# Kernel tuning notes

Measured on AMD Instinct MI355X. Metric: run time of the kernel, lower is better.

## Reference

```python
import jax, jax.numpy as jnp
import numpy as np

N_NODES = 100000
N_EDGES = 3200000
N_GRAPHS = 128
IN_DIM = 4
HID = 64
BN_EPS = 1e-5


def setup_inputs() -> dict:
    key = jax.random.key(0)
    ks = jax.random.split(key, 24)
    x = jax.random.normal(ks[0], (N_NODES, IN_DIM), dtype=jnp.float32)
    edge_index = jax.random.randint(ks[1], (2, N_EDGES), 0, N_NODES, dtype=jnp.int32)
    batch_ids = jnp.sort(jax.random.randint(ks[2], (N_NODES,), 0, N_GRAPHS, dtype=jnp.int32))

    def lin(k, out_d, in_d):
        s = 1.0 / np.sqrt(in_d)
        return jax.random.uniform(k, (out_d, in_d), jnp.float32, -s, s)

    inp = {
        'x': x, 'edge_index': edge_index, 'batch_ids': batch_ids,
        # SAGEConv i: out = lin_l(mean_neighbors) + lin_r(x_self); bias lives in lin_l
        'w1l': lin(ks[3], HID, IN_DIM), 'b1': jnp.zeros((HID,), jnp.float32), 'w1r': lin(ks[4], HID, IN_DIM),
        'bn1_g': jnp.ones((HID,), jnp.float32), 'bn1_b': jnp.zeros((HID,), jnp.float32),
        'w2l': lin(ks[5], HID, HID), 'b2': jnp.zeros((HID,), jnp.float32), 'w2r': lin(ks[6], HID, HID),
        'bn2_g': jnp.ones((HID,), jnp.float32), 'bn2_b': jnp.zeros((HID,), jnp.float32),
        'w3l': lin(ks[7], HID, HID), 'b3': jnp.zeros((HID,), jnp.float32), 'w3r': lin(ks[8], HID, HID),
        'bn3_g': jnp.ones((HID,), jnp.float32), 'bn3_b': jnp.zeros((HID,), jnp.float32),
        'fc1_w': lin(ks[9], 64, HID), 'fc1_b': jnp.zeros((64,), jnp.float32),
        'fc2_w': lin(ks[10], 2, 64), 'fc2_b': jnp.zeros((2,), jnp.float32),
    }
    return inp


def _sage(x, src, dst, deg_inv, wl, bl, wr):
    # mean-aggregate neighbor messages (source -> target), then two small GEMMs
    msum = jax.ops.segment_sum(x[src], dst, num_segments=N_NODES)  # [N, d]
    agg = msum * deg_inv[:, None]
    return agg @ wl.T + bl + x @ wr.T


def _bn(x, g, b):
    # BatchNorm1d in training mode: batch stats over node dim, biased variance
    m = jnp.mean(x, axis=0)
    v = jnp.mean((x - m) ** 2, axis=0)
    return (x - m) * jax.lax.rsqrt(v + BN_EPS) * g + b


def reference(x, edge_index, batch_ids,
              w1l, b1, w1r, bn1_g, bn1_b,
              w2l, b2, w2r, bn2_g, bn2_b,
              w3l, b3, w3r, bn3_g, bn3_b,
              fc1_w, fc1_b, fc2_w, fc2_b):
    src, dst = edge_index[0], edge_index[1]
    deg = jax.ops.segment_sum(jnp.ones((src.shape[0],), x.dtype), dst, num_segments=N_NODES)
    deg_inv = 1.0 / jnp.maximum(deg, 1.0)

    h = jax.nn.relu(_bn(_sage(x, src, dst, deg_inv, w1l, b1, w1r), bn1_g, bn1_b))
    h = jax.nn.relu(_bn(_sage(h, src, dst, deg_inv, w2l, b2, w2r), bn2_g, bn2_b))
    h = jax.nn.relu(_bn(_sage(h, src, dst, deg_inv, w3l, b3, w3r), bn3_g, bn3_b))

    # global_mean_pool over graphs
    gsum = jax.ops.segment_sum(h, batch_ids, num_segments=N_GRAPHS)
    gcnt = jax.ops.segment_sum(jnp.ones((h.shape[0],), h.dtype), batch_ids, num_segments=N_GRAPHS)
    pooled = gsum / jnp.maximum(gcnt, 1.0)[:, None]

    # MLP head (dropout = identity at inference)
    hid = jax.nn.relu(pooled @ fc1_w.T + fc1_b)
    return hid @ fc2_w.T + fc2_b
```

## Files before the change

kernel.cpp:

```cpp
#include <hip/hip_runtime.h>
#include <hip/hip_fp16.h>

#define NN 100000
#define NE 3200000
#define NG 128
#define BN_EPS 1e-5f

#define NBUK 782
#define BSHIFT 7
#define BCAP 6144

#define GRID_SG 1024
#define PBMAX 2048
#define PSLICE 8

typedef _Float16 h2v __attribute__((ext_vector_type(2)));
typedef unsigned int u32x2 __attribute__((ext_vector_type(2)));
typedef unsigned int u32x4 __attribute__((ext_vector_type(4)));


__global__ void __launch_bounds__(512) k_scatter(
    const int* __restrict__ src, const int* __restrict__ dst,
    int* __restrict__ slab_cursor, unsigned int* __restrict__ slab, int E) {
    __shared__ int hist[NBUK + 2];
    __shared__ int cbase[NBUK + 2];
    int tid = threadIdx.x;
    int eBeg = blockIdx.x * 12500;
    int eEnd = min(eBeg + 12500, E);

    for (int t = tid; t < NBUK; t += 512) hist[t] = 0;
    __syncthreads();
    for (int e = eBeg + tid; e < eEnd; e += 512) {
        int b = dst[e] >> BSHIFT;
        atomicAdd(&hist[b], 1);
    }
    __syncthreads();
    for (int t = tid; t < NBUK; t += 512) {
        int c = hist[t];
        cbase[t] = (c > 0) ? atomicAdd(&slab_cursor[t], c) : 0;
    }
    __syncthreads();
    for (int t = tid; t < NBUK; t += 512) hist[t] = 0;
    __syncthreads();
    for (int e = eBeg + tid; e < eEnd; e += 512) {
        int d = dst[e];
        int b = d >> BSHIFT;
        int r = atomicAdd(&hist[b], 1);
        int pos = cbase[b] + r;
        if (pos < BCAP) slab[(size_t)b * BCAP + pos] = ((unsigned)src[e] << BSHIFT) | (unsigned)(d & 127);
    }
}

__global__ void __launch_bounds__(512) k_bucket_csr(
    const unsigned int* __restrict__ slab, const int* __restrict__ slab_cursor,
    int* __restrict__ row_ptr,
    float* __restrict__ deg_inv, int* __restrict__ csr_src,
    const float* __restrict__ x, const float* __restrict__ w1l,
    const float* __restrict__ b1, const float* __restrict__ w1r,
    __half* __restrict__ hp16, float* __restrict__ part) {
    __shared__ int lds_csr[BCAP];
    __shared__ int red[512];
    __shared__ int sdeg[128];
    __shared__ int sscan[128];
    __shared__ int slcur[128];
    __shared__ float swl[256], swr[256], sb1[64];
    __shared__ float ssum[64], ssq[64];
    int tid = threadIdx.x;
    int b = blockIdx.x;
    int lo = b << BSHIFT;
    int cnt = min(slab_cursor[b], BCAP);
    const unsigned int* sl = slab + (size_t)b * BCAP;

    int partial = 0;
    for (int j = tid; j < b; j += 512) partial += min(slab_cursor[j], BCAP);
    red[tid] = partial;
    __syncthreads();
    for (int off = 256; off > 0; off >>= 1) {
        if (tid < off) red[tid] += red[tid + off];
        __syncthreads();
    }
    int base = red[0];
    if (b == NBUK - 1 && tid == 0) row_ptr[NN] = base + cnt;

    if (tid < 256) { swl[tid] = w1l[tid]; swr[tid] = w1r[tid]; }
    if (tid < 64)  { sb1[tid] = b1[tid]; ssum[tid] = 0.f; ssq[tid] = 0.f; }
    if (tid < 128) sdeg[tid] = 0;
    __syncthreads();

    unsigned int myv[12];
    int mycount = 0;
    for (int k = tid; k < cnt; k += 512) myv[mycount++] = sl[k];
#pragma unroll
    for (int j = 0; j < 12; j++)
        if (j < mycount) atomicAdd(&sdeg[myv[j] & 127], 1);
    __syncthreads();
    int v = (tid < 128) ? sdeg[tid] : 0;
    if (tid < 128) sscan[tid] = v;
    __syncthreads();
    for (int off = 1; off < 128; off <<= 1) {
        int add = 0;
        if (tid < 128 && tid >= off) add = sscan[tid - off];
        __syncthreads();
        if (tid < 128) sscan[tid] += add;
        __syncthreads();
    }
    if (tid < 128) {
        int excl = sscan[tid] - v;
        int n = lo + tid;
        if (n < NN) {
            row_ptr[n] = base + excl;
            deg_inv[n] = 1.0f / fmaxf((float)v, 1.0f);
        }
        slcur[tid] = excl;
    }
    __syncthreads();
#pragma unroll
    for (int j = 0; j < 12; j++)
        if (j < mycount) {
            unsigned int p = myv[j];
            int pos = atomicAdd(&slcur[p & 127], 1);
            lds_csr[pos] = (int)(p >> BSHIFT);
        }
    __syncthreads();
    for (int k = tid; k < cnt; k += 512) csr_src[base + k] = lds_csr[k];

    int i = tid >> 2, c = tid & 3;
    int n = lo + i;
    bool valid = (n < NN);
    int dhi = sscan[i];
    int dlo = dhi - sdeg[i];
    const float4* x4 = (const float4*)x;
    float4 acc = make_float4(0.f, 0.f, 0.f, 0.f);
    int k = dlo + c;
    for (; k + 12 < dhi; k += 16) {
        int s0 = lds_csr[k], s1 = lds_csr[k + 4], s2 = lds_csr[k + 8], s3 = lds_csr[k + 12];
        float4 v0 = x4[s0];
        float4 v1 = x4[s1];
        float4 v2 = x4[s2];
        float4 v3 = x4[s3];
        acc.x += v0.x + v1.x + v2.x + v3.x;
        acc.y += v0.y + v1.y + v2.y + v3.y;
        acc.z += v0.z + v1.z + v2.z + v3.z;
        acc.w += v0.w + v1.w + v2.w + v3.w;
    }
    for (; k < dhi; k += 4) {
        int s = lds_csr[k];
        float4 xv = x4[s];
        acc.x += xv.x; acc.y += xv.y; acc.z += xv.z; acc.w += xv.w;
    }
#pragma unroll
    for (int m = 1; m <= 2; m <<= 1) {
        acc.x += __shfl_xor(acc.x, m);
        acc.y += __shfl_xor(acc.y, m);
        acc.z += __shfl_xor(acc.z, m);
        acc.w += __shfl_xor(acc.w, m);
    }
    float dv = 1.0f / fmaxf((float)sdeg[i], 1.0f);
    float ax = acc.x * dv, ay = acc.y * dv, az = acc.z * dv, aw = acc.w * dv;
    float4 xs = valid ? x4[n] : make_float4(0.f, 0.f, 0.f, 0.f);

#pragma unroll
    for (int m4 = 0; m4 < 4; m4++) {
        float4 o = make_float4(0.f, 0.f, 0.f, 0.f);
        float* op = &o.x;
        if (valid) {
#pragma unroll
            for (int t = 0; t < 4; t++) {
                int j = c * 16 + m4 * 4 + t;
                float s = sb1[j];
                s += ax * swl[j * 4 + 0] + ay * swl[j * 4 + 1] + az * swl[j * 4 + 2] + aw * swl[j * 4 + 3];
                s += xs.x * swr[j * 4 + 0] + xs.y * swr[j * 4 + 1] + xs.z * swr[j * 4 + 2] + xs.w * swr[j * 4 + 3];
                op[t] = s;
            }
            h2v p0 = h2v{(_Float16)o.x, (_Float16)o.y};
            h2v p1 = h2v{(_Float16)o.z, (_Float16)o.w};
            u32x2 w;
            w.x = *(unsigned int*)&p0;
            w.y = *(unsigned int*)&p1;
            __builtin_nontemporal_store(w, (u32x2*)hp16 + (size_t)n * 16 + c * 4 + m4);
        }
        float4 q = make_float4(o.x * o.x, o.y * o.y, o.z * o.z, o.w * o.w);
#pragma unroll
        for (int m = 4; m <= 32; m <<= 1) {
            o.x += __shfl_xor(o.x, m); o.y += __shfl_xor(o.y, m);
            o.z += __shfl_xor(o.z, m); o.w += __shfl_xor(o.w, m);
            q.x += __shfl_xor(q.x, m); q.y += __shfl_xor(q.y, m);
            q.z += __shfl_xor(q.z, m); q.w += __shfl_xor(q.w, m);
        }
        if ((tid & 63) < 4) {
            int jb = c * 16 + m4 * 4;
            atomicAdd(&ssum[jb + 0], o.x); atomicAdd(&ssum[jb + 1], o.y);
            atomicAdd(&ssum[jb + 2], o.z); atomicAdd(&ssum[jb + 3], o.w);
            atomicAdd(&ssq[jb + 0], q.x);  atomicAdd(&ssq[jb + 1], q.y);
            atomicAdd(&ssq[jb + 2], q.z);  atomicAdd(&ssq[jb + 3], q.w);
        }
    }
    __syncthreads();
    if (tid < 64) {
        part[(2 * tid) * PBMAX + blockIdx.x]     = ssum[tid];
        part[(2 * tid + 1) * PBMAX + blockIdx.x] = ssq[tid];
    }
}

__global__ void __launch_bounds__(512, 8) k_sage(
    const __half* __restrict__ h_in, const float* __restrict__ sbv_in,
    const int* __restrict__ row_ptr,
    const int* __restrict__ csr_src, const float* __restrict__ deg_inv,
    const float* __restrict__ wl, const float* __restrict__ bl,
    const float* __restrict__ wr, __half* __restrict__ hp16,
    float* __restrict__ part) {
    __shared__ h2v wl2s[32][68];
    __shared__ h2v wr2s[32][68];
    __shared__ h2v tAh[32][36];
    __shared__ h2v tXh[32][36];
    __shared__ float ssum[64], ssq[64];
    int tid = threadIdx.x;
    for (int idx = tid; idx < 2048; idx += 512) {
        int j = idx & 63, kk = idx >> 6;
        float2 l = ((const float2*)wl)[j * 32 + kk];
        float2 r = ((const float2*)wr)[j * 32 + kk];
        wl2s[kk][j] = h2v{(_Float16)l.x, (_Float16)l.y};
        wr2s[kk][j] = h2v{(_Float16)r.x, (_Float16)r.y};
    }
    if (tid < 64) { ssum[tid] = 0.f; ssq[tid] = 0.f; }
    __syncthreads();

    int g = tid & 15, ni = tid >> 4;
    h2v sch0 = h2v{(_Float16)sbv_in[4 * g + 0], (_Float16)sbv_in[4 * g + 1]};
    h2v sch1 = h2v{(_Float16)sbv_in[4 * g + 2], (_Float16)sbv_in[4 * g + 3]};
    h2v bih0 = h2v{(_Float16)sbv_in[64 + 4 * g + 0], (_Float16)sbv_in[64 + 4 * g + 1]};
    h2v bih1 = h2v{(_Float16)sbv_in[64 + 4 * g + 2], (_Float16)sbv_in[64 + 4 * g + 3]};
    h2v hz = h2v{(_Float16)0.f, (_Float16)0.f};

    const uint2* tbl = (const uint2*)h_in;
    const int ntiles = NN / 32;

#define BN_ACC_H(vv) { \
        h2v a0 = *(h2v*)&vv.x, a1 = *(h2v*)&vv.y; \
        hacc0 += __builtin_elementwise_max(a0 * sch0 + bih0, hz); \
        hacc1 += __builtin_elementwise_max(a1 * sch1 + bih1, hz); }

    for (int tile = blockIdx.x; tile < ntiles; tile += GRID_SG) {
        int n = tile * 32 + ni;
        float ax = 0.f, ay = 0.f, az = 0.f, aw = 0.f;
        int r0 = row_ptr[n], r1 = row_ptr[n + 1];
        int e = r0;
        for (; e + 8 <= r1; e += 8) {
            int s0 = csr_src[e],     s1 = csr_src[e + 1], s2 = csr_src[e + 2], s3 = csr_src[e + 3];
            int s4 = csr_src[e + 4], s5 = csr_src[e + 5], s6 = csr_src[e + 6], s7 = csr_src[e + 7];
            uint2 v0 = tbl[(size_t)s0 * 16 + g];
            uint2 v1 = tbl[(size_t)s1 * 16 + g];
            uint2 v2 = tbl[(size_t)s2 * 16 + g];
            uint2 v3 = tbl[(size_t)s3 * 16 + g];
            uint2 v4 = tbl[(size_t)s4 * 16 + g];
            uint2 v5 = tbl[(size_t)s5 * 16 + g];
            uint2 v6 = tbl[(size_t)s6 * 16 + g];
            uint2 v7 = tbl[(size_t)s7 * 16 + g];
            h2v hacc0 = hz, hacc1 = hz;
            BN_ACC_H(v0) BN_ACC_H(v1) BN_ACC_H(v2) BN_ACC_H(v3)
            BN_ACC_H(v4) BN_ACC_H(v5) BN_ACC_H(v6) BN_ACC_H(v7)
            ax += (float)hacc0.x; ay += (float)hacc0.y;
            az += (float)hacc1.x; aw += (float)hacc1.y;
        }
        for (; e < r1; ++e) {
            int s = csr_src[e];
            uint2 vv = tbl[(size_t)s * 16 + g];
            h2v a0 = *(h2v*)&vv.x, a1 = *(h2v*)&vv.y;
            a0 = __builtin_elementwise_max(a0 * sch0 + bih0, hz);
            a1 = __builtin_elementwise_max(a1 * sch1 + bih1, hz);
            ax += (float)a0.x; ay += (float)a0.y; az += (float)a1.x; aw += (float)a1.y;
        }
        float di = deg_inv[n];
        uint2 rsv = tbl[(size_t)n * 16 + g];
        h2v xs0h = __builtin_elementwise_max(*(h2v*)&rsv.x * sch0 + bih0, hz);
        h2v xs1h = __builtin_elementwise_max(*(h2v*)&rsv.y * sch1 + bih1, hz);
        ax *= di; ay *= di; az *= di; aw *= di;
        tAh[ni][2 * g]     = h2v{(_Float16)ax, (_Float16)ay};
        tAh[ni][2 * g + 1] = h2v{(_Float16)az, (_Float16)aw};
        tXh[ni][2 * g]     = xs0h;
        tXh[ni][2 * g + 1] = xs1h;
        __syncthreads();

        float4 o = ((const float4*)bl)[g];
#pragma unroll 4
        for (int kk = 0; kk < 32; kk++) {
            h2v a2 = tAh[ni][kk];
            h2v x2 = tXh[ni][kk];
            h2v l0 = wl2s[kk][4 * g + 0], l1 = wl2s[kk][4 * g + 1];
            h2v l2 = wl2s[kk][4 * g + 2], l3 = wl2s[kk][4 * g + 3];
            h2v r0v = wr2s[kk][4 * g + 0], r1v = wr2s[kk][4 * g + 1];
            h2v r2v = wr2s[kk][4 * g + 2], r3v = wr2s[kk][4 * g + 3];
#if __has_builtin(__builtin_amdgcn_fdot2)
            o.x = __builtin_amdgcn_fdot2(a2, l0, o.x, false);
            o.y = __builtin_amdgcn_fdot2(a2, l1, o.y, false);
            o.z = __builtin_amdgcn_fdot2(a2, l2, o.z, false);
            o.w = __builtin_amdgcn_fdot2(a2, l3, o.w, false);
            o.x = __builtin_amdgcn_fdot2(x2, r0v, o.x, false);
            o.y = __builtin_amdgcn_fdot2(x2, r1v, o.y, false);
            o.z = __builtin_amdgcn_fdot2(x2, r2v, o.z, false);
            o.w = __builtin_amdgcn_fdot2(x2, r3v, o.w, false);
#else
            float b0 = (float)a2.x, b1 = (float)a2.y, x0 = (float)x2.x, x1 = (float)x2.y;
            o.x += b0 * (float)l0.x + b1 * (float)l0.y + x0 * (float)r0v.x + x1 * (float)r0v.y;
            o.y += b0 * (float)l1.x + b1 * (float)l1.y + x0 * (float)r1v.x + x1 * (float)r1v.y;
            o.z += b0 * (float)l2.x + b1 * (float)l2.y + x0 * (float)r2v.x + x1 * (float)r2v.y;
            o.w += b0 * (float)l3.x + b1 * (float)l3.y + x0 * (float)r3v.x + x1 * (float)r3v.y;
#endif
        }
        {
            h2v p0 = h2v{(_Float16)o.x, (_Float16)o.y};
            h2v p1 = h2v{(_Float16)o.z, (_Float16)o.w};
            u32x2 w;
            w.x = *(unsigned int*)&p0;
            w.y = *(unsigned int*)&p1;
            __builtin_nontemporal_store(w, (u32x2*)hp16 + (size_t)n * 16 + g);
        }

        float4 qv = make_float4(o.x * o.x, o.y * o.y, o.z * o.z, o.w * o.w);
#pragma unroll
        for (int m = 16; m <= 32; m <<= 1) {
            o.x += __shfl_xor(o.x, m); o.y += __shfl_xor(o.y, m);
            o.z += __shfl_xor(o.z, m); o.w += __shfl_xor(o.w, m);
            qv.x += __shfl_xor(qv.x, m); qv.y += __shfl_xor(qv.y, m);
            qv.z += __shfl_xor(qv.z, m); qv.w += __shfl_xor(qv.w, m);
        }
        if ((tid & 48) == 0) {
            atomicAdd(&ssum[4 * g + 0], o.x); atomicAdd(&ssum[4 * g + 1], o.y);
            atomicAdd(&ssum[4 * g + 2], o.z); atomicAdd(&ssum[4 * g + 3], o.w);
            atomicAdd(&ssq[4 * g + 0], qv.x);  atomicAdd(&ssq[4 * g + 1], qv.y);
            atomicAdd(&ssq[4 * g + 2], qv.z);  atomicAdd(&ssq[4 * g + 3], qv.w);
        }
        __syncthreads();
    }
#undef BN_ACC_H
    if (tid < 64) {
        part[(2 * tid) * PBMAX + blockIdx.x]     = ssum[tid];
        part[(2 * tid + 1) * PBMAX + blockIdx.x] = ssq[tid];
    }
}

__global__ void k_reduce_sb(const float* __restrict__ part, int PB,
                            const float* __restrict__ gamma, const float* __restrict__ beta,
                            float* __restrict__ sbv, int N) {
    int c = blockIdx.x;
    float s = 0.f, q = 0.f;
    for (int b = threadIdx.x; b < PB; b += 256) {
        s += part[(2 * c) * PBMAX + b];
        q += part[(2 * c + 1) * PBMAX + b];
    }
    __shared__ float rs[256], rq[256];
    rs[threadIdx.x] = s;
    rq[threadIdx.x] = q;
    __syncthreads();
    for (int off = 128; off > 0; off >>= 1) {
        if (threadIdx.x < off) {
            rs[threadIdx.x] += rs[threadIdx.x + off];
            rq[threadIdx.x] += rq[threadIdx.x + off];
        }
        __syncthreads();
    }
    if (threadIdx.x == 0) {
        float m = rs[0] / (float)N;
        float var = rq[0] / (float)N - m * m;
        float sc = gamma[c] * rsqrtf(var + BN_EPS);
        sbv[c]      = sc;
        sbv[64 + c] = beta[c] - m * sc;
    }
}

__global__ void __launch_bounds__(256) k_pool_partial(
    const __half* __restrict__ hp16, const float* __restrict__ sbv,
    const int* __restrict__ batch, float* __restrict__ pooled_part, int N) {
    __shared__ float ssc[64], sbi[64];
    __shared__ float sm[256];
    if (threadIdx.x < 64) {
        ssc[threadIdx.x] = sbv[threadIdx.x];
        sbi[threadIdx.x] = sbv[64 + threadIdx.x];
    }
    __syncthreads();
    int gph = blockIdx.x >> 3;
    int slice = blockIdx.x & 7;
    int lo = 0, hi = N;
    while (lo < hi) { int mid = (lo + hi) >> 1; if (batch[mid] < gph) lo = mid + 1; else hi = mid; }
    int start = lo;
    hi = N;
    while (lo < hi) { int mid = (lo + hi) >> 1; if (batch[mid] < gph + 1) lo = mid + 1; else hi = mid; }
    int end = lo;

    int c = threadIdx.x & 63, w = threadIdx.x >> 6;
    float s = 0.f;
    for (int r = start + slice * 4 + w; r < end; r += 32)
        s += fmaxf(__half2float(hp16[(size_t)r * 64 + c]) * ssc[c] + sbi[c], 0.f);
    sm[threadIdx.x] = s;
    __syncthreads();
    if (threadIdx.x < 64) {
        float t = sm[c] + sm[64 + c] + sm[128 + c] + sm[192 + c];
        pooled_part[(size_t)(gph * PSLICE + slice) * 64 + c] = t;
    }
}

__global__ void __launch_bounds__(64) k_head(
    const float* __restrict__ pooled_part, const int* __restrict__ batch,
    const float* __restrict__ fc1w, const float* __restrict__ fc1b,
    const float* __restrict__ fc2w, const float* __restrict__ fc2b,
    float* __restrict__ out, int N) {
    __shared__ float pl[64], hid[64];
    int gph = blockIdx.x;
    int j = threadIdx.x;
    int lo = 0, hi = N;
    while (lo < hi) { int mid = (lo + hi) >> 1; if (batch[mid] < gph) lo = mid + 1; else hi = mid; }
    int start = lo;
    hi = N;
    while (lo < hi) { int mid = (lo + hi) >> 1; if (batch[mid] < gph + 1) lo = mid + 1; else hi = mid; }
    int cnt = lo - start;

    float t = 0.f;
#pragma unroll
    for (int s = 0; s < PSLICE; s++) t += pooled_part[(size_t)(gph * PSLICE + s) * 64 + j];
    pl[j] = t / fmaxf((float)cnt, 1.0f);
    __syncthreads();
    float v = fc1b[j];
    for (int k = 0; k < 64; k++) v += pl[k] * fc1w[j * 64 + k];
    hid[j] = fmaxf(v, 0.f);
    __syncthreads();
    if (j < 2) {
        float o = fc2b[j];
        for (int k = 0; k < 64; k++) o += hid[k] * fc2w[j * 64 + k];
        out[gph * 2 + j] = o;
    }
}

extern "C" void kernel_launch(void* const* d_in, const int* in_sizes, int n_in,
                              void* d_out, int out_size, void* d_ws, size_t ws_size,
                              hipStream_t stream) {
    const float* x    = (const float*)d_in[0];
    const int* ei     = (const int*)d_in[1];
    const int* batch  = (const int*)d_in[2];
    const float* w1l  = (const float*)d_in[3];
    const float* b1   = (const float*)d_in[4];
    const float* w1r  = (const float*)d_in[5];
    const float* bn1g = (const float*)d_in[6];
    const float* bn1b = (const float*)d_in[7];
    const float* w2l  = (const float*)d_in[8];
    const float* b2   = (const float*)d_in[9];
    const float* w2r  = (const float*)d_in[10];
    const float* bn2g = (const float*)d_in[11];
    const float* bn2b = (const float*)d_in[12];
    const float* w3l  = (const float*)d_in[13];
    const float* b3   = (const float*)d_in[14];
    const float* w3r  = (const float*)d_in[15];
    const float* bn3g = (const float*)d_in[16];
    const float* bn3b = (const float*)d_in[17];
    const float* fc1w = (const float*)d_in[18];
    const float* fc1b = (const float*)d_in[19];
    const float* fc2w = (const float*)d_in[20];
    const float* fc2b = (const float*)d_in[21];
    float* out = (float*)d_out;

    const int N = NN, E = NE;
    const int* srcp = ei;
    const int* dstp = ei + E;

    char* ws = (char*)d_ws;
    size_t off = 0;
    auto alloc = [&](size_t bytes) -> char* {
        char* p = ws + off;
        off += (bytes + 255) & ~(size_t)255;
        return p;
    };
    int* csr_src       = (int*)alloc(sizeof(int) * E);
    __half* hpA        = (__half*)alloc(sizeof(__half) * N * 64);
    __half* hpB        = (__half*)alloc(sizeof(__half) * N * 64);
    unsigned int* slab = (unsigned int*)alloc(sizeof(unsigned int) * (size_t)NBUK * BCAP);
    int* slab_cursor   = (int*)alloc(sizeof(int) * NBUK);
    int* row_ptr       = (int*)alloc(sizeof(int) * (N + 1));
    float* deg_inv     = (float*)alloc(sizeof(float) * N);
    float* part        = (float*)alloc(sizeof(float) * 128 * PBMAX);
    float* sbv         = (float*)alloc(sizeof(float) * 128);
    float* pooled_part = (float*)alloc(sizeof(float) * NG * PSLICE * 64);

    hipMemsetAsync(slab_cursor, 0, sizeof(int) * NBUK, stream);

    k_scatter<<<256, 512, 0, stream>>>(srcp, dstp, slab_cursor, slab, E);
    k_bucket_csr<<<NBUK, 512, 0, stream>>>(slab, slab_cursor, row_ptr, deg_inv,
                                           csr_src, x, w1l, b1, w1r, hpA, part);
    k_reduce_sb<<<64, 256, 0, stream>>>(part, NBUK, bn1g, bn1b, sbv, N);

    k_sage<<<GRID_SG, 512, 0, stream>>>(hpA, sbv, row_ptr, csr_src, deg_inv,
                                        w2l, b2, w2r, hpB, part);
    k_reduce_sb<<<64, 256, 0, stream>>>(part, GRID_SG, bn2g, bn2b, sbv, N);

    k_sage<<<GRID_SG, 512, 0, stream>>>(hpB, sbv, row_ptr, csr_src, deg_inv,
                                        w3l, b3, w3r, hpA, part);
    k_reduce_sb<<<64, 256, 0, stream>>>(part, GRID_SG, bn3g, bn3b, sbv, N);

    k_pool_partial<<<NG * PSLICE, 256, 0, stream>>>(hpA, sbv, batch, pooled_part, N);
    k_head<<<NG, 64, 0, stream>>>(pooled_part, batch, fc1w, fc1b, fc2w, fc2b, out, N);
}
```

Measured before the change: 380.4 us.

## Stage per-tile CSR source indices in LDS and widen the gather unroll

Each block cooperatively loads the CSR source indices for its 32-node tile into a shared buffer with coalesced reads. It prefetches the next tile's indices after the tile barrier, so the per-thread gather reads indices from LDS rather than global memory. The gather loop is unrolled to 16 loads with 32-bit byte-offset addressing, which adds memory-level parallelism. The cost is 12 KB of extra LDS per block, which can reduce occupancy. Tiles with more edges than fit the buffer fall back to global index reads.

```diff
diff --git a/kernel.cpp b/kernel.cpp
--- a/kernel.cpp
+++ b/kernel.cpp
@@ -13,6 +13,7 @@
 #define GRID_SG 1024
 #define PBMAX 2048
 #define PSLICE 8
+#define ECAP 3072
 
 typedef _Float16 h2v __attribute__((ext_vector_type(2)));
 typedef unsigned int u32x2 __attribute__((ext_vector_type(2)));
@@ -214,6 +215,7 @@
     __shared__ h2v tAh[32][36];
     __shared__ h2v tXh[32][36];
     __shared__ float ssum[64], ssq[64];
+    __shared__ int lds_e[ECAP];
     int tid = threadIdx.x;
     for (int idx = tid; idx < 2048; idx += 512) {
         int j = idx & 63, kk = idx >> 6;
@@ -223,55 +225,85 @@
         wr2s[kk][j] = h2v{(_Float16)r.x, (_Float16)r.y};
     }
     if (tid < 64) { ssum[tid] = 0.f; ssq[tid] = 0.f; }
-    __syncthreads();
 
     int g = tid & 15, ni = tid >> 4;
+    unsigned g8 = (unsigned)(g << 3);
     h2v sch0 = h2v{(_Float16)sbv_in[4 * g + 0], (_Float16)sbv_in[4 * g + 1]};
     h2v sch1 = h2v{(_Float16)sbv_in[4 * g + 2], (_Float16)sbv_in[4 * g + 3]};
     h2v bih0 = h2v{(_Float16)sbv_in[64 + 4 * g + 0], (_Float16)sbv_in[64 + 4 * g + 1]};
     h2v bih1 = h2v{(_Float16)sbv_in[64 + 4 * g + 2], (_Float16)sbv_in[64 + 4 * g + 3]};
     h2v hz = h2v{(_Float16)0.f, (_Float16)0.f};
 
-    const uint2* tbl = (const uint2*)h_in;
+    const char* hb = (const char*)h_in;
     const int ntiles = NN / 32;
+
+    int tile = blockIdx.x;
+    int ebase = row_ptr[tile << 5];
+    int ecnt  = min(row_ptr[(tile << 5) + 32] - ebase, ECAP);
+    for (int i = tid; i < ecnt; i += 512) lds_e[i] = csr_src[ebase + i];
+    __syncthreads();
 
 #define BN_ACC_H(vv) { \
         h2v a0 = *(h2v*)&vv.x, a1 = *(h2v*)&vv.y; \
         hacc0 += __builtin_elementwise_max(a0 * sch0 + bih0, hz); \
         hacc1 += __builtin_elementwise_max(a1 * sch1 + bih1, hz); }
 
-    for (int tile = blockIdx.x; tile < ntiles; tile += GRID_SG) {
-        int n = tile * 32 + ni;
+    for (; tile < ntiles; tile += GRID_SG) {
+        int n = (tile << 5) + ni;
         float ax = 0.f, ay = 0.f, az = 0.f, aw = 0.f;
-        int r0 = row_ptr[n], r1 = row_ptr[n + 1];
+        int r0 = row_ptr[n] - ebase, r1 = row_ptr[n + 1] - ebase;
+        int rL = min(r1, ecnt);
         int e = r0;
-        for (; e + 8 <= r1; e += 8) {
-            int s0 = csr_src[e],     s1 = csr_src[e + 1], s2 = csr_src[e + 2], s3 = csr_src[e + 3];
-            int s4 = csr_src[e + 4], s5 = csr_src[e + 5], s6 = csr_src[e + 6], s7 = csr_src[e + 7];
-            uint2 v0 = tbl[(size_t)s0 * 16 + g];
-            uint2 v1 = tbl[(size_t)s1 * 16 + g];
-            uint2 v2 = tbl[(size_t)s2 * 16 + g];
-            uint2 v3 = tbl[(size_t)s3 * 16 + g];
-            uint2 v4 = tbl[(size_t)s4 * 16 + g];
-            uint2 v5 = tbl[(size_t)s5 * 16 + g];
-            uint2 v6 = tbl[(size_t)s6 * 16 + g];
-            uint2 v7 = tbl[(size_t)s7 * 16 + g];
+        for (; e + 16 <= rL; e += 16) {
+            uint2 v[16];
+#pragma unroll
+            for (int k = 0; k < 16; k++) {
+                unsigned off = ((unsigned)lds_e[e + k] << 7) | g8;
+                v[k] = *(const uint2*)(hb + off);
+            }
             h2v hacc0 = hz, hacc1 = hz;
-            BN_ACC_H(v0) BN_ACC_H(v1) BN_ACC_H(v2) BN_ACC_H(v3)
-            BN_ACC_H(v4) BN_ACC_H(v5) BN_ACC_H(v6) BN_ACC_H(v7)
+#pragma unroll
+            for (int k = 0; k < 8; k++) BN_ACC_H(v[k])
             ax += (float)hacc0.x; ay += (float)hacc0.y;
             az += (float)hacc1.x; aw += (float)hacc1.y;
-        }
-        for (; e < r1; ++e) {
-            int s = csr_src[e];
-            uint2 vv = tbl[(size_t)s * 16 + g];
+            hacc0 = hz; hacc1 = hz;
+#pragma unroll
+            for (int k = 8; k < 16; k++) BN_ACC_H(v[k])
+            ax += (float)hacc0.x; ay += (float)hacc0.y;
+            az += (float)hacc1.x; aw += (float)hacc1.y;
+        }
+        if (e + 8 <= rL) {
+            uint2 v[8];
+#pragma unroll
+            for (int k = 0; k < 8; k++) {
+                unsigned off = ((unsigned)lds_e[e + k] << 7) | g8;
+                v[k] = *(const uint2*)(hb + off);
+            }
+            h2v hacc0 = hz, hacc1 = hz;
+#pragma unroll
+            for (int k = 0; k < 8; k++) BN_ACC_H(v[k])
+            ax += (float)hacc0.x; ay += (float)hacc0.y;
+            az += (float)hacc1.x; aw += (float)hacc1.y;
+            e += 8;
+        }
+        for (; e < rL; ++e) {
+            unsigned off = ((unsigned)lds_e[e] << 7) | g8;
+            uint2 vv = *(const uint2*)(hb + off);
             h2v a0 = *(h2v*)&vv.x, a1 = *(h2v*)&vv.y;
             a0 = __builtin_elementwise_max(a0 * sch0 + bih0, hz);
             a1 = __builtin_elementwise_max(a1 * sch1 + bih1, hz);
             ax += (float)a0.x; ay += (float)a0.y; az += (float)a1.x; aw += (float)a1.y;
         }
+        for (; e < r1; ++e) {
+            unsigned off = ((unsigned)csr_src[ebase + e] << 7) | g8;
+            uint2 vv = *(const uint2*)(hb + off);
+            h2v a0 = *(h2v*)&vv.x, a1 = *(h2v*)&vv.y;
+            a0 = __builtin_elementwise_max(a0 * sch0 + bih0, hz);
+            a1 = __builtin_elementwise_max(a1 * sch1 + bih1, hz);
+            ax += (float)a0.x; ay += (float)a0.y; az += (float)a1.x; aw += (float)a1.y;
+        }
         float di = deg_inv[n];
-        uint2 rsv = tbl[(size_t)n * 16 + g];
+        uint2 rsv = *(const uint2*)(hb + (((unsigned)n << 7) | g8));
         h2v xs0h = __builtin_elementwise_max(*(h2v*)&rsv.x * sch0 + bih0, hz);
         h2v xs1h = __builtin_elementwise_max(*(h2v*)&rsv.y * sch1 + bih1, hz);
         ax *= di; ay *= di; az *= di; aw *= di;
@@ -280,6 +312,14 @@
         tXh[ni][2 * g]     = xs0h;
         tXh[ni][2 * g + 1] = xs1h;
         __syncthreads();
+
+        int tile2 = tile + GRID_SG;
+        if (tile2 < ntiles) {
+            int eb2 = row_ptr[tile2 << 5];
+            int ec2 = min(row_ptr[(tile2 << 5) + 32] - eb2, ECAP);
+            for (int i = tid; i < ec2; i += 512) lds_e[i] = csr_src[eb2 + i];
+            ebase = eb2; ecnt = ec2;
+        }
 
         float4 o = ((const float4*)bl)[g];
 #pragma unroll 4
```

Result: slower. 388.1 us (+2.0%).

## Precompute BN+ReLU activations once per node instead of per gathered edge

Applied to the files above, without the earlier changes.

Adds a k_bnact pass that applies batch-norm scale/bias and ReLU to each node's fp16 features once, writing them into the reused slab buffer. The SAGE kernel then gathers the already-activated rows and only sums them, dropping the per-edge FMA and max work across 32 gathers per node. It also switches to byte-offset address math and 128-bit LDS loads for the small GEMM. The cost is an extra full read and write of the 100k x 64 fp16 feature array plus one more kernel launch per layer.

```diff
diff --git a/kernel.cpp b/kernel.cpp
--- a/kernel.cpp
+++ b/kernel.cpp
@@ -17,6 +17,13 @@
 typedef _Float16 h2v __attribute__((ext_vector_type(2)));
 typedef unsigned int u32x2 __attribute__((ext_vector_type(2)));
 typedef unsigned int u32x4 __attribute__((ext_vector_type(4)));
+
+static __device__ __forceinline__ h2v as_h2(unsigned int u) {
+    return __builtin_bit_cast(h2v, u);
+}
+static __device__ __forceinline__ unsigned int as_u32(h2v h) {
+    return __builtin_bit_cast(unsigned int, h);
+}
 
 
 __global__ void __launch_bounds__(512) k_scatter(
@@ -202,8 +209,38 @@
     }
 }
 
+__global__ void __launch_bounds__(256) k_bnact(
+    const __half* __restrict__ hp, const float* __restrict__ sbv,
+    __half* __restrict__ ha) {
+    __shared__ float s_sc[64], s_bi[64];
+    int tid = threadIdx.x;
+    if (tid < 64) { s_sc[tid] = sbv[tid]; s_bi[tid] = sbv[64 + tid]; }
+    __syncthreads();
+    int c = tid & 7;
+    h2v sc[4], bi[4];
+#pragma unroll
+    for (int j = 0; j < 4; j++) {
+        sc[j] = h2v{(_Float16)s_sc[8 * c + 2 * j], (_Float16)s_sc[8 * c + 2 * j + 1]};
+        bi[j] = h2v{(_Float16)s_bi[8 * c + 2 * j], (_Float16)s_bi[8 * c + 2 * j + 1]};
+    }
+    h2v hz = h2v{(_Float16)0.f, (_Float16)0.f};
+    const u32x4* in4 = (const u32x4*)hp;
+    u32x4* out4 = (u32x4*)ha;
+    const int total = NN * 8;
+    for (int i = blockIdx.x * 256 + tid; i < total; i += gridDim.x * 256) {
+        u32x4 v = in4[i];
+#pragma unroll
+        for (int j = 0; j < 4; j++) {
+            h2v a = as_h2(v[j]);
+            a = __builtin_elementwise_max(a * sc[j] + bi[j], hz);
+            v[j] = as_u32(a);
+        }
+        out4[i] = v;
+    }
+}
+
 __global__ void __launch_bounds__(512, 8) k_sage(
-    const __half* __restrict__ h_in, const float* __restrict__ sbv_in,
+    const __half* __restrict__ h_act,
     const int* __restrict__ row_ptr,
     const int* __restrict__ csr_src, const float* __restrict__ deg_inv,
     const float* __restrict__ wl, const float* __restrict__ bl,
@@ -226,86 +263,87 @@
     __syncthreads();
 
     int g = tid & 15, ni = tid >> 4;
-    h2v sch0 = h2v{(_Float16)sbv_in[4 * g + 0], (_Float16)sbv_in[4 * g + 1]};
-    h2v sch1 = h2v{(_Float16)sbv_in[4 * g + 2], (_Float16)sbv_in[4 * g + 3]};
-    h2v bih0 = h2v{(_Float16)sbv_in[64 + 4 * g + 0], (_Float16)sbv_in[64 + 4 * g + 1]};
-    h2v bih1 = h2v{(_Float16)sbv_in[64 + 4 * g + 2], (_Float16)sbv_in[64 + 4 * g + 3]};
+    unsigned g8 = (unsigned)(g << 3);
     h2v hz = h2v{(_Float16)0.f, (_Float16)0.f};
-
-    const uint2* tbl = (const uint2*)h_in;
+    const char* hb = (const char*)h_act;
     const int ntiles = NN / 32;
-
-#define BN_ACC_H(vv) { \
-        h2v a0 = *(h2v*)&vv.x, a1 = *(h2v*)&vv.y; \
-        hacc0 += __builtin_elementwise_max(a0 * sch0 + bih0, hz); \
-        hacc1 += __builtin_elementwise_max(a1 * sch1 + bih1, hz); }
+    float4 bo = ((const float4*)bl)[g];
 
     for (int tile = blockIdx.x; tile < ntiles; tile += GRID_SG) {
-        int n = tile * 32 + ni;
+        int n = (tile << 5) + ni;
+        int r0 = row_ptr[n], r1 = row_ptr[n + 1];
+        float di = deg_inv[n];
+        uint2 rsv = *(const uint2*)(hb + (((unsigned)n << 7) | g8));
         float ax = 0.f, ay = 0.f, az = 0.f, aw = 0.f;
-        int r0 = row_ptr[n], r1 = row_ptr[n + 1];
         int e = r0;
         for (; e + 8 <= r1; e += 8) {
             int s0 = csr_src[e],     s1 = csr_src[e + 1], s2 = csr_src[e + 2], s3 = csr_src[e + 3];
             int s4 = csr_src[e + 4], s5 = csr_src[e + 5], s6 = csr_src[e + 6], s7 = csr_src[e + 7];
-            uint2 v0 = tbl[(size_t)s0 * 16 + g];
-            uint2 v1 = tbl[(size_t)s1 * 16 + g];
-            uint2 v2 = tbl[(size_t)s2 * 16 + g];
-            uint2 v3 = tbl[(size_t)s3 * 16 + g];
-            uint2 v4 = tbl[(size_t)s4 * 16 + g];
-            uint2 v5 = tbl[(size_t)s5 * 16 + g];
-            uint2 v6 = tbl[(size_t)s6 * 16 + g];
-            uint2 v7 = tbl[(size_t)s7 * 16 + g];
+            uint2 v0 = *(const uint2*)(hb + (((unsigned)s0 << 7) | g8));
+            uint2 v1 = *(const uint2*)(hb + (((unsigned)s1 << 7) | g8));
+            uint2 v2 = *(const uint2*)(hb + (((unsigned)s2 << 7) | g8));
+            uint2 v3 = *(const uint2*)(hb + (((unsigned)s3 << 7) | g8));
+            uint2 v4 = *(const uint2*)(hb + (((unsigned)s4 << 7) | g8));
+            uint2 v5 = *(const uint2*)(hb + (((unsigned)s5 << 7) | g8));
+            uint2 v6 = *(const uint2*)(hb + (((unsigned)s6 << 7) | g8));
+            uint2 v7 = *(const uint2*)(hb + (((unsigned)s7 << 7) | g8));
             h2v hacc0 = hz, hacc1 = hz;
-            BN_ACC_H(v0) BN_ACC_H(v1) BN_ACC_H(v2) BN_ACC_H(v3)
-            BN_ACC_H(v4) BN_ACC_H(v5) BN_ACC_H(v6) BN_ACC_H(v7)
+            hacc0 += as_h2(v0.x); hacc1 += as_h2(v0.y);
+            hacc0 += as_h2(v1.x); hacc1 += as_h2(v1.y);
+            hacc0 += as_h2(v2.x); hacc1 += as_h2(v2.y);
+            hacc0 += as_h2(v3.x); hacc1 += as_h2(v3.y);
+            hacc0 += as_h2(v4.x); hacc1 += as_h2(v4.y);
+            hacc0 += as_h2(v5.x); hacc1 += as_h2(v5.y);
+            hacc0 += as_h2(v6.x); hacc1 += as_h2(v6.y);
+            hacc0 += as_h2(v7.x); hacc1 += as_h2(v7.y);
             ax += (float)hacc0.x; ay += (float)hacc0.y;
             az += (float)hacc1.x; aw += (float)hacc1.y;
         }
         for (; e < r1; ++e) {
             int s = csr_src[e];
-            uint2 vv = tbl[(size_t)s * 16 + g];
-            h2v a0 = *(h2v*)&vv.x, a1 = *(h2v*)&vv.y;
-            a0 = __builtin_elementwise_max(a0 * sch0 + bih0, hz);
-            a1 = __builtin_elementwise_max(a1 * sch1 + bih1, hz);
+            uint2 vv = *(const uint2*)(hb + (((unsigned)s << 7) | g8));
+            h2v a0 = as_h2(vv.x), a1 = as_h2(vv.y);
             ax += (float)a0.x; ay += (float)a0.y; az += (float)a1.x; aw += (float)a1.y;
         }
-        float di = deg_inv[n];
-        uint2 rsv = tbl[(size_t)n * 16 + g];
-        h2v xs0h = __builtin_elementwise_max(*(h2v*)&rsv.x * sch0 + bih0, hz);
-        h2v xs1h = __builtin_elementwise_max(*(h2v*)&rsv.y * sch1 + bih1, hz);
         ax *= di; ay *= di; az *= di; aw *= di;
         tAh[ni][2 * g]     = h2v{(_Float16)ax, (_Float16)ay};
         tAh[ni][2 * g + 1] = h2v{(_Float16)az, (_Float16)aw};
-        tXh[ni][2 * g]     = xs0h;
-        tXh[ni][2 * g + 1] = xs1h;
+        tXh[ni][2 * g]     = as_h2(rsv.x);
+        tXh[ni][2 * g + 1] = as_h2(rsv.y);
         __syncthreads();
 
-        float4 o = ((const float4*)bl)[g];
-#pragma unroll 4
-        for (int kk = 0; kk < 32; kk++) {
-            h2v a2 = tAh[ni][kk];
-            h2v x2 = tXh[ni][kk];
-            h2v l0 = wl2s[kk][4 * g + 0], l1 = wl2s[kk][4 * g + 1];
-            h2v l2 = wl2s[kk][4 * g + 2], l3 = wl2s[kk][4 * g + 3];
-            h2v r0v = wr2s[kk][4 * g + 0], r1v = wr2s[kk][4 * g + 1];
-            h2v r2v = wr2s[kk][4 * g + 2], r3v = wr2s[kk][4 * g + 3];
+        float4 o = bo;
+#pragma unroll
+        for (int kk = 0; kk < 32; kk += 4) {
+            u32x4 av = *(const u32x4*)&tAh[ni][kk];
+            u32x4 xv = *(const u32x4*)&tXh[ni][kk];
+#pragma unroll
+            for (int j = 0; j < 4; j++) {
+                u32x4 wlv = *(const u32x4*)&wl2s[kk + j][4 * g];
+                u32x4 wrv = *(const u32x4*)&wr2s[kk + j][4 * g];
+                h2v a2 = as_h2(av[j]);
+                h2v x2 = as_h2(xv[j]);
 #if __has_builtin(__builtin_amdgcn_fdot2)
-            o.x = __builtin_amdgcn_fdot2(a2, l0, o.x, false);
-            o.y = __builtin_amdgcn_fdot2(a2, l1, o.y, false);
-            o.z = __builtin_amdgcn_fdot2(a2, l2, o.z, false);
-            o.w = __builtin_amdgcn_fdot2(a2, l3, o.w, false);
-            o.x = __builtin_amdgcn_fdot2(x2, r0v, o.x, false);
-            o.y = __builtin_amdgcn_fdot2(x2, r1v, o.y, false);
-            o.z = __builtin_amdgcn_fdot2(x2, r2v, o.z, false);
-            o.w = __builtin_amdgcn_fdot2(x2, r3v, o.w, false);
+                o.x = __builtin_amdgcn_fdot2(a2, as_h2(wlv[0]), o.x, false);
+                o.y = __builtin_amdgcn_fdot2(a2, as_h2(wlv[1]), o.y, false);
+                o.z = __builtin_amdgcn_fdot2(a2, as_h2(wlv[2]), o.z, false);
+                o.w = __builtin_amdgcn_fdot2(a2, as_h2(wlv[3]), o.w, false);
+                o.x = __builtin_amdgcn_fdot2(x2, as_h2(wrv[0]), o.x, false);
+                o.y = __builtin_amdgcn_fdot2(x2, as_h2(wrv[1]), o.y, false);
+                o.z = __builtin_amdgcn_fdot2(x2, as_h2(wrv[2]), o.z, false);
+                o.w = __builtin_amdgcn_fdot2(x2, as_h2(wrv[3]), o.w, false);
 #else
-            float b0 = (float)a2.x, b1 = (float)a2.y, x0 = (float)x2.x, x1 = (float)x2.y;
-            o.x += b0 * (float)l0.x + b1 * (float)l0.y + x0 * (float)r0v.x + x1 * (float)r0v.y;
-            o.y += b0 * (float)l1.x + b1 * (float)l1.y + x0 * (float)r1v.x + x1 * (float)r1v.y;
-            o.z += b0 * (float)l2.x + b1 * (float)l2.y + x0 * (float)r2v.x + x1 * (float)r2v.y;
-            o.w += b0 * (float)l3.x + b1 * (float)l3.y + x0 * (float)r3v.x + x1 * (float)r3v.y;
+                {
+                    h2v l0 = as_h2(wlv[0]), l1 = as_h2(wlv[1]), l2 = as_h2(wlv[2]), l3 = as_h2(wlv[3]);
+                    h2v q0 = as_h2(wrv[0]), q1 = as_h2(wrv[1]), q2 = as_h2(wrv[2]), q3 = as_h2(wrv[3]);
+                    float b0 = (float)a2.x, b1 = (float)a2.y, x0 = (float)x2.x, x1 = (float)x2.y;
+                    o.x += b0 * (float)l0.x + b1 * (float)l0.y + x0 * (float)q0.x + x1 * (float)q0.y;
+                    o.y += b0 * (float)l1.x + b1 * (float)l1.y + x0 * (float)q1.x + x1 * (float)q1.y;
+                    o.z += b0 * (float)l2.x + b1 * (float)l2.y + x0 * (float)q2.x + x1 * (float)q2.y;
+                    o.w += b0 * (float)l3.x + b1 * (float)l3.y + x0 * (float)q3.x + x1 * (float)q3.y;
+                }
 #endif
+            }
         }
         {
             h2v p0 = h2v{(_Float16)o.x, (_Float16)o.y};
@@ -332,7 +370,6 @@
         }
         __syncthreads();
     }
-#undef BN_ACC_H
     if (tid < 64) {
         part[(2 * tid) * PBMAX + blockIdx.x]     = ssum[tid];
         part[(2 * tid + 1) * PBMAX + blockIdx.x] = ssq[tid];
@@ -479,6 +516,8 @@
     float* sbv         = (float*)alloc(sizeof(float) * 128);
     float* pooled_part = (float*)alloc(sizeof(float) * NG * PSLICE * 64);
 
+    __half* hAct = (__half*)slab;
+
     hipMemsetAsync(slab_cursor, 0, sizeof(int) * NBUK, stream);
 
     k_scatter<<<256, 512, 0, stream>>>(srcp, dstp, slab_cursor, slab, E);
@@ -486,11 +525,13 @@
                                            csr_src, x, w1l, b1, w1r, hpA, part);
     k_reduce_sb<<<64, 256, 0, stream>>>(part, NBUK, bn1g, bn1b, sbv, N);
 
-    k_sage<<<GRID_SG, 512, 0, stream>>>(hpA, sbv, row_ptr, csr_src, deg_inv,
+    k_bnact<<<1024, 256, 0, stream>>>(hpA, sbv, hAct);
+    k_sage<<<GRID_SG, 512, 0, stream>>>(hAct, row_ptr, csr_src, deg_inv,
                                         w2l, b2, w2r, hpB, part);
     k_reduce_sb<<<64, 256, 0, stream>>>(part, GRID_SG, bn2g, bn2b, sbv, N);
 
-    k_sage<<<GRID_SG, 512, 0, stream>>>(hpB, sbv, row_ptr, csr_src, deg_inv,
+    k_bnact<<<1024, 256, 0, stream>>>(hpB, sbv, hAct);
+    k_sage<<<GRID_SG, 512, 0, stream>>>(hAct, row_ptr, csr_src, deg_inv,
                                         w3l, b3, w3r, hpA, part);
     k_reduce_sb<<<64, 256, 0, stream>>>(part, GRID_SG, bn3g, bn3b, sbv, N);
 
```

New measurement: 390.0 us. 1.03x slower.
